# Performance work log

Hardware: AMD Instinct MI355X
Metric: run time of the kernel (lower is better)

Reference implementation:

```python
import jax, jax.numpy as jnp
import numpy as np

N_NODES = 100000
N_EDGES = 1600000
IN_C, HID_C, OUT_C, N_CLS = 64, 128, 64, 20


def setup_inputs() -> dict:
    key = jax.random.key(0)
    ks = jax.random.split(key, 8)
    s = lambda k, sh: jax.random.normal(k, sh, dtype=jnp.float32) * (1.0 / np.sqrt(sh[0]))
    return {
        "x": jax.random.normal(ks[0], (N_NODES, IN_C), dtype=jnp.float32),
        "edge_index": jax.random.randint(ks[1], (2, N_EDGES), 0, N_NODES, dtype=jnp.int64),
        "w_self1": s(ks[2], (IN_C, HID_C)),
        "w_neigh1": s(ks[3], (IN_C, HID_C)),
        "b1": jnp.zeros((HID_C,), dtype=jnp.float32),
        "w_self2": s(ks[4], (HID_C, OUT_C)),
        "w_neigh2": s(ks[5], (HID_C, OUT_C)),
        "b2": jnp.zeros((OUT_C,), dtype=jnp.float32),
        "wc": s(ks[6], (OUT_C, N_CLS)),
        "bc": jnp.zeros((N_CLS,), dtype=jnp.float32),
    }


def _sage_mean(feat, src, dst, deg_inv, w_self, w_neigh, b):
    # gather messages along edges, segment-sum at destinations, mean-normalize
    msg_sum = jax.ops.segment_sum(feat[src], dst, num_segments=N_NODES)  # [N, d]
    h_neigh = msg_sum * deg_inv[:, None]
    return feat @ w_self + h_neigh @ w_neigh + b


def reference(x, edge_index, w_self1, w_neigh1, b1, w_self2, w_neigh2, b2, wc, bc):
    src, dst = edge_index[0], edge_index[1]
    deg = jax.ops.segment_sum(jnp.ones((src.shape[0],), dtype=x.dtype), dst,
                              num_segments=N_NODES)
    deg_inv = 1.0 / jnp.maximum(deg, 1.0)  # zero-degree nodes -> 0 neighbor mean
    h = jax.nn.relu(_sage_mean(x, src, dst, deg_inv, w_self1, w_neigh1, b1))
    h = jax.nn.relu(_sage_mean(h, src, dst, deg_inv, w_self2, w_neigh2, b2))
    return h @ wc + bc
```

## Files before the change

### kernel.cpp

```cpp
#include <hip/hip_runtime.h>

#define N_NODES 100000
#define N_EDGES 1600000
#define IN_C    64
#define HID_C   128
#define OUT_C   64
#define N_CLS   20

#define BUCKETS 196
#define XSL     8
#define WCAP    2560
#define EPB     4096
#define CAPB    44

typedef __attribute__((ext_vector_type(8))) short short8;
typedef __attribute__((ext_vector_type(4))) float floatx4;

__device__ __forceinline__ unsigned short f2bf(float f) {
    union { float f; unsigned u; } v; v.f = f;
    unsigned r = v.u + 0x7FFFu + ((v.u >> 16) & 1u);
    return (unsigned short)(r >> 16);
}
__device__ __forceinline__ unsigned pk2(float lo, float hi) {
    return (unsigned)f2bf(lo) | ((unsigned)f2bf(hi) << 16);
}
__device__ __forceinline__ float bflo(unsigned w) { return __uint_as_float(w << 16); }
__device__ __forceinline__ float bfhi(unsigned w) { return __uint_as_float(w & 0xFFFF0000u); }

__global__ __launch_bounds__(256) void binA_kernel(
        const int* __restrict__ ei, int* __restrict__ bcnt,
        unsigned* __restrict__ bins)
{
    __shared__ unsigned lbins[BUCKETS * CAPB];
    __shared__ unsigned comp[EPB];
    __shared__ unsigned dsti[EPB];
    __shared__ int lcnt[BUCKETS], lofs[BUCKETS], gb[BUCKETS];
    __shared__ int sd[256];

    const int tid = threadIdx.x;
    const int xcd = blockIdx.x & (XSL - 1);
    const int e0  = blockIdx.x * EPB;

    for (int w = tid; w < BUCKETS; w += 256) lcnt[w] = 0;
    __syncthreads();

    for (int it = 0; it < EPB / 256; ++it) {
        int e = e0 + it * 256 + tid;
        if (e >= N_EDGES) break;
        int src = ei[e];
        int dst = ei[N_EDGES + e];
        int b = dst >> 9;
        unsigned pk = ((unsigned)(dst & 511) << 17) | (unsigned)src;
        int pos = atomicAdd(&lcnt[b], 1);
        if (pos < CAPB) {
            lbins[b * CAPB + pos] = pk;
        } else {
            int gp = atomicAdd(&bcnt[b * XSL + xcd], 1);
            if (gp < WCAP)
                bins[(unsigned)(b * XSL + xcd) * WCAP + gp] = pk;
        }
    }
    __syncthreads();

    int c = (tid < BUCKETS) ? min(lcnt[tid], CAPB) : 0;
    sd[tid] = c;
    __syncthreads();
    for (int off = 1; off < 256; off <<= 1) {
        int x = 0;
        if (tid >= off) x = sd[tid - off];
        __syncthreads();
        if (tid >= off) sd[tid] += x;
        __syncthreads();
    }
    if (tid < BUCKETS) lofs[tid] = sd[tid] - c;
    __syncthreads();
    const int T = sd[255];

    if (tid < BUCKETS) {
        int cw = min(lcnt[tid], CAPB);
        gb[tid] = (cw > 0) ? atomicAdd(&bcnt[tid * XSL + xcd], cw) : 0;
    }
    __syncthreads();

    if (tid < BUCKETS) {
        int cw = min(lcnt[tid], CAPB);
        int lo = lofs[tid];
        unsigned wb = (unsigned)(tid * XSL + xcd) * WCAP + (unsigned)gb[tid];
        for (int i = 0; i < cw; ++i) {
            comp[lo + i] = lbins[tid * CAPB + i];
            dsti[lo + i] = wb + i;
        }
    }
    __syncthreads();

    for (int i = tid; i < T; i += 256)
        bins[dsti[i]] = comp[i];
}

__global__ __launch_bounds__(256) void bscan_kernel(
        const int* __restrict__ bcnt, int* __restrict__ bucket_base,
        int* __restrict__ row_ptr)
{
    __shared__ int sd[256];
    int t = threadIdx.x;
    int tot = 0;
    if (t < BUCKETS) {
        for (int sl = 0; sl < XSL; ++sl)
            tot += min(bcnt[t * XSL + sl], WCAP);
    }
    sd[t] = tot;
    __syncthreads();
    for (int off = 1; off < 256; off <<= 1) {
        int x = 0;
        if (t >= off) x = sd[t - off];
        __syncthreads();
        if (t >= off) sd[t] += x;
        __syncthreads();
    }
    if (t < BUCKETS) bucket_base[t] = sd[t] - tot;
    if (t == 0) row_ptr[N_NODES] = N_EDGES;
}

__global__ __launch_bounds__(256) void buildB_kernel(
        const int* __restrict__ bcnt, const unsigned* __restrict__ bins,
        const int* __restrict__ bucket_base,
        int* __restrict__ row_ptr, int* __restrict__ sorted_src,
        float* __restrict__ dinv)
{
    __shared__ unsigned ent[16384];
    __shared__ int scnt[XSL], soff[XSL];
    __shared__ int cnt[512], lofs[512], cur[512];
    __shared__ int sd[256];

    const int b   = blockIdx.x;
    const int tid = threadIdx.x;
    const int node0 = b * 512;

    if (tid < XSL) scnt[tid] = min(bcnt[b * XSL + tid], WCAP);
    { int i = tid; cnt[i] = 0; cnt[i + 256] = 0; }
    __syncthreads();
    if (tid == 0) {
        int acc = 0;
        for (int sl = 0; sl < XSL; ++sl) {
            soff[sl] = acc;
            acc += scnt[sl];
            if (acc > 16384) { scnt[sl] -= (acc - 16384); acc = 16384; }
        }
    }
    __syncthreads();

    for (int sl = 0; sl < XSL; ++sl) {
        int len = scnt[sl];
        const unsigned* seg = bins + (unsigned)(b * XSL + sl) * WCAP;
        int base = soff[sl];
        for (int i = tid; i < len; i += 256) {
            unsigned e = seg[i];
            ent[base + i] = e;
            atomicAdd((unsigned*)&cnt[e >> 17], 1u);
        }
    }
    __syncthreads();
    const int T = soff[XSL - 1] + scnt[XSL - 1];

    int a0 = cnt[2 * tid], a1 = cnt[2 * tid + 1];
    int s2 = a0 + a1;
    sd[tid] = s2;
    __syncthreads();
    for (int off = 1; off < 256; off <<= 1) {
        int x = 0;
        if (tid >= off) x = sd[tid - off];
        __syncthreads();
        if (tid >= off) sd[tid] += x;
        __syncthreads();
    }
    int excl = sd[tid] - s2;
    lofs[2 * tid]     = excl;
    lofs[2 * tid + 1] = excl + a0;
    cur[2 * tid]      = excl;
    cur[2 * tid + 1]  = excl + a0;
    __syncthreads();

    const int gbase = bucket_base[b];
    for (int j = tid; j < 512; j += 256) {
        int node = node0 + j;
        if (node < N_NODES) {
            row_ptr[node] = gbase + lofs[j];
            dinv[node] = 1.0f / (float)max(cnt[j], 1);
        }
    }
    for (int i = tid; i < T; i += 256) {
        unsigned e = ent[i];
        int dl = e >> 17;
        int p = atomicAdd((unsigned*)&cur[dl], 1u);
        sorted_src[gbase + p] = (int)(e & 0x1FFFFu);
    }
}


__global__ __launch_bounds__(256) void cvt_x_kernel(
        const float* __restrict__ x, unsigned short* __restrict__ xb)
{
    int i = blockIdx.x * 256 + threadIdx.x;
    if (i >= N_NODES * 64 / 8) return;
    float4 a = ((const float4*)x)[(size_t)i * 2];
    float4 b = ((const float4*)x)[(size_t)i * 2 + 1];
    uint4 r;
    r.x = pk2(a.x, a.y); r.y = pk2(a.z, a.w);
    r.z = pk2(b.x, b.y); r.w = pk2(b.z, b.w);
    ((uint4*)xb)[i] = r;
}

__global__ __launch_bounds__(256) void prep_wt_kernel(
        const float* __restrict__ ws1, const float* __restrict__ wn1,
        const float* __restrict__ ws2, const float* __restrict__ wn2,
        unsigned short* __restrict__ wt1s, unsigned short* __restrict__ wt1n,
        unsigned short* __restrict__ wt2s, unsigned short* __restrict__ wt2n)
{
    int i = blockIdx.x * 256 + threadIdx.x;
    if (i < 8192) {
        int o = i >> 6, c = i & 63;
        wt1s[i] = f2bf(ws1[c * 128 + o]);
        wt1n[i] = f2bf(wn1[c * 128 + o]);
    } else if (i < 16384) {
        int j = i - 8192;
        int o = j >> 7, c = j & 127;
        wt2s[j] = f2bf(ws2[c * 64 + o]);
        wt2n[j] = f2bf(wn2[c * 64 + o]);
    }
}

__global__ __launch_bounds__(256) void gatherb_kernel(
        const int* __restrict__ row_ptr, const int* __restrict__ srcs,
        const unsigned short* __restrict__ featb,
        const float* __restrict__ dinv, unsigned short* __restrict__ aggb)
{
    int gid = blockIdx.x * 256 + threadIdx.x;
    int n = gid >> 3;
    int q = gid & 7;
    if (n >= N_NODES) return;
    int beg = row_ptr[n];
    int end = row_ptr[n + 1];
    const uint4* f4 = (const uint4*)featb;
    float a0=0,a1=0,a2=0,a3=0,a4=0,a5=0,a6=0,a7=0;
    int e = beg;
    for (; e + 4 <= end; e += 4) {
        int s0 = srcs[e], s1 = srcs[e+1], s2 = srcs[e+2], s3 = srcs[e+3];
        uint4 v0 = f4[(size_t)s0 * 8 + q];
        uint4 v1 = f4[(size_t)s1 * 8 + q];
        uint4 v2 = f4[(size_t)s2 * 8 + q];
        uint4 v3 = f4[(size_t)s3 * 8 + q];
        a0 += bflo(v0.x); a1 += bfhi(v0.x); a2 += bflo(v0.y); a3 += bfhi(v0.y);
        a4 += bflo(v0.z); a5 += bfhi(v0.z); a6 += bflo(v0.w); a7 += bfhi(v0.w);
        a0 += bflo(v1.x); a1 += bfhi(v1.x); a2 += bflo(v1.y); a3 += bfhi(v1.y);
        a4 += bflo(v1.z); a5 += bfhi(v1.z); a6 += bflo(v1.w); a7 += bfhi(v1.w);
        a0 += bflo(v2.x); a1 += bfhi(v2.x); a2 += bflo(v2.y); a3 += bfhi(v2.y);
        a4 += bflo(v2.z); a5 += bfhi(v2.z); a6 += bflo(v2.w); a7 += bfhi(v2.w);
        a0 += bflo(v3.x); a1 += bfhi(v3.x); a2 += bflo(v3.y); a3 += bfhi(v3.y);
        a4 += bflo(v3.z); a5 += bfhi(v3.z); a6 += bflo(v3.w); a7 += bfhi(v3.w);
    }
    for (; e < end; ++e) {
        uint4 v = f4[(size_t)srcs[e] * 8 + q];
        a0 += bflo(v.x); a1 += bfhi(v.x); a2 += bflo(v.y); a3 += bfhi(v.y);
        a4 += bflo(v.z); a5 += bfhi(v.z); a6 += bflo(v.w); a7 += bfhi(v.w);
    }
    float di = dinv[n];
    uint4 r;
    r.x = pk2(a0 * di, a1 * di);
    r.y = pk2(a2 * di, a3 * di);
    r.z = pk2(a4 * di, a5 * di);
    r.w = pk2(a6 * di, a7 * di);
    ((uint4*)aggb)[(size_t)n * 8 + q] = r;
}


__global__ __launch_bounds__(256) void dense1_mfma(
        const unsigned short* __restrict__ xb,
        const unsigned short* __restrict__ aggb,
        const unsigned short* __restrict__ wts,
        const unsigned short* __restrict__ wtn,
        const float* __restrict__ bias,
        unsigned short* __restrict__ h1b)
{
    int lane = threadIdx.x & 63;
    int wv   = threadIdx.x >> 6;
    int quad = lane >> 4;
    int col  = lane & 15;
    int nl = blockIdx.x * 64 + wv * 16 + col;
    int nc = min(nl, N_NODES - 1);
    bool ok = nl < N_NODES;

    const short8 bs0 = *(const short8*)(xb   + (size_t)nc * 64 +      quad * 8);
    const short8 bs1 = *(const short8*)(xb   + (size_t)nc * 64 + 32 + quad * 8);
    const short8 bn0 = *(const short8*)(aggb + (size_t)nc * 64 +      quad * 8);
    const short8 bn1 = *(const short8*)(aggb + (size_t)nc * 64 + 32 + quad * 8);

#pragma unroll
    for (int mt = 0; mt < 8; ++mt) {
        int m = mt * 16 + col;
        const short8 as0 = *(const short8*)(wts + (size_t)m * 64 +      quad * 8);
        const short8 as1 = *(const short8*)(wts + (size_t)m * 64 + 32 + quad * 8);
        const short8 an0 = *(const short8*)(wtn + (size_t)m * 64 +      quad * 8);
        const short8 an1 = *(const short8*)(wtn + (size_t)m * 64 + 32 + quad * 8);
        floatx4 acc = {0.f, 0.f, 0.f, 0.f};
        acc = __builtin_amdgcn_mfma_f32_16x16x32_bf16(as0, bs0, acc, 0, 0, 0);
        acc = __builtin_amdgcn_mfma_f32_16x16x32_bf16(as1, bs1, acc, 0, 0, 0);
        acc = __builtin_amdgcn_mfma_f32_16x16x32_bf16(an0, bn0, acc, 0, 0, 0);
        acc = __builtin_amdgcn_mfma_f32_16x16x32_bf16(an1, bn1, acc, 0, 0, 0);
        if (ok) {
            int och = mt * 16 + quad * 4;
            float4 bv = *(const float4*)(bias + och);
            ushort4 r;
            r.x = f2bf(fmaxf(acc[0] + bv.x, 0.f));
            r.y = f2bf(fmaxf(acc[1] + bv.y, 0.f));
            r.z = f2bf(fmaxf(acc[2] + bv.z, 0.f));
            r.w = f2bf(fmaxf(acc[3] + bv.w, 0.f));
            *(ushort4*)(h1b + (size_t)nl * 128 + och) = r;
        }
    }
}

__global__ __launch_bounds__(256) void t2_mfma(
        const unsigned short* __restrict__ h1b,
        const unsigned short* __restrict__ wtn,
        unsigned short* __restrict__ t2b)
{
    int lane = threadIdx.x & 63;
    int wv   = threadIdx.x >> 6;
    int quad = lane >> 4;
    int col  = lane & 15;
    int nl = blockIdx.x * 64 + wv * 16 + col;
    int nc = min(nl, N_NODES - 1);
    bool ok = nl < N_NODES;

    short8 b[4];
#pragma unroll
    for (int kc = 0; kc < 4; ++kc)
        b[kc] = *(const short8*)(h1b + (size_t)nc * 128 + kc * 32 + quad * 8);

#pragma unroll
    for (int mt = 0; mt < 4; ++mt) {
        int m = mt * 16 + col;
        floatx4 acc = {0.f, 0.f, 0.f, 0.f};
#pragma unroll
        for (int kc = 0; kc < 4; ++kc) {
            const short8 a = *(const short8*)(wtn + (size_t)m * 128 + kc * 32 + quad * 8);
            acc = __builtin_amdgcn_mfma_f32_16x16x32_bf16(a, b[kc], acc, 0, 0, 0);
        }
        if (ok) {
            int och = mt * 16 + quad * 4;
            ushort4 r;
            r.x = f2bf(acc[0]); r.y = f2bf(acc[1]);
            r.z = f2bf(acc[2]); r.w = f2bf(acc[3]);
            *(ushort4*)(t2b + (size_t)nl * 64 + och) = r;
        }
    }
}

__global__ __launch_bounds__(256) void dense2_cls_mfma(
        const unsigned short* __restrict__ h1b,
        const unsigned short* __restrict__ wts,
        const unsigned short* __restrict__ agg2b,
        const float* __restrict__ b2,
        const float* __restrict__ wc,
        const float* __restrict__ bc,
        float* __restrict__ out)
{
    __shared__ float hs[64][65];
    __shared__ float wcs[64 * N_CLS];
    __shared__ float bcs[N_CLS];

    int tid = threadIdx.x;
    int lane = tid & 63;
    int wv   = tid >> 6;
    int quad = lane >> 4;
    int col  = lane & 15;
    int node0 = blockIdx.x * 64;
    int nl = node0 + wv * 16 + col;
    int nc = min(nl, N_NODES - 1);

    for (int t = tid; t < 64 * N_CLS; t += 256) wcs[t] = wc[t];
    if (tid < N_CLS) bcs[tid] = bc[tid];

    short8 b[4];
#pragma unroll
    for (int kc = 0; kc < 4; ++kc)
        b[kc] = *(const short8*)(h1b + (size_t)nc * 128 + kc * 32 + quad * 8);

#pragma unroll
    for (int mt = 0; mt < 4; ++mt) {
        int m = mt * 16 + col;
        floatx4 acc = {0.f, 0.f, 0.f, 0.f};
#pragma unroll
        for (int kc = 0; kc < 4; ++kc) {
            const short8 a = *(const short8*)(wts + (size_t)m * 128 + kc * 32 + quad * 8);
            acc = __builtin_amdgcn_mfma_f32_16x16x32_bf16(a, b[kc], acc, 0, 0, 0);
        }
        int och = mt * 16 + quad * 4;
        ushort4 au = *(const ushort4*)(agg2b + (size_t)nc * 64 + och);
        float4 bv = *(const float4*)(b2 + och);
        hs[wv * 16 + col][och + 0] = fmaxf(acc[0] + __uint_as_float((unsigned)au.x << 16) + bv.x, 0.f);
        hs[wv * 16 + col][och + 1] = fmaxf(acc[1] + __uint_as_float((unsigned)au.y << 16) + bv.y, 0.f);
        hs[wv * 16 + col][och + 2] = fmaxf(acc[2] + __uint_as_float((unsigned)au.z << 16) + bv.z, 0.f);
        hs[wv * 16 + col][och + 3] = fmaxf(acc[3] + __uint_as_float((unsigned)au.w << 16) + bv.w, 0.f);
    }
    __syncthreads();

    for (int o = tid; o < 64 * N_CLS; o += 256) {
        int n = o / N_CLS, cls = o % N_CLS;
        if (node0 + n >= N_NODES) continue;
        float s = bcs[cls];
#pragma unroll
        for (int k = 0; k < 64; ++k) s += hs[n][k] * wcs[k * N_CLS + cls];
        out[(size_t)(node0 + n) * N_CLS + cls] = s;
    }
}


extern "C" void kernel_launch(void* const* d_in, const int* in_sizes, int n_in,
                              void* d_out, int out_size, void* d_ws, size_t ws_size,
                              hipStream_t stream)
{
    const float* x        = (const float*)d_in[0];
    const int*   ei       = (const int*)  d_in[1];
    const float* w_self1  = (const float*)d_in[2];
    const float* w_neigh1 = (const float*)d_in[3];
    const float* b1       = (const float*)d_in[4];
    const float* w_self2  = (const float*)d_in[5];
    const float* w_neigh2 = (const float*)d_in[6];
    const float* b2       = (const float*)d_in[7];
    const float* wc       = (const float*)d_in[8];
    const float* bc       = (const float*)d_in[9];
    float* out = (float*)d_out;

    const size_t N = N_NODES;
    int*      bcnt    = (int*)d_ws;
    int*      bbase   = bcnt + BUCKETS * XSL;
    int*      row_ptr = bbase + 200;
    unsigned* bins    = (unsigned*)(row_ptr + N + 8);
    int*      s_src   = (int*)(bins + BUCKETS * XSL * WCAP);
    float*    dinv    = (float*)(s_src + N_EDGES);
    unsigned short* xb    = (unsigned short*)(dinv + N);
    unsigned short* agg1b = xb + 64 * N;
    unsigned short* h1b   = agg1b + 64 * N;
    unsigned short* t2b   = h1b + 128 * N;
    unsigned short* agg2b = t2b + 64 * N;
    unsigned short* wt1s  = agg2b + 64 * N;
    unsigned short* wt1n  = wt1s + 8192;
    unsigned short* wt2s  = wt1n + 8192;
    unsigned short* wt2n  = wt2s + 8192;

    hipMemsetAsync(bcnt, 0, BUCKETS * XSL * sizeof(int), stream);

    const int EB2 = (N_EDGES + EPB - 1) / EPB;
    const int GB = (N_NODES * 8) / 256;
    const int MB = (N_NODES + 63) / 64;

    cvt_x_kernel<<<(N_NODES * 64 / 8 + 255) / 256, 256, 0, stream>>>(x, xb);
    prep_wt_kernel<<<64, 256, 0, stream>>>(w_self1, w_neigh1, w_self2, w_neigh2,
                                           wt1s, wt1n, wt2s, wt2n);

    binA_kernel<<<EB2, 256, 0, stream>>>(ei, bcnt, bins);
    bscan_kernel<<<1, 256, 0, stream>>>(bcnt, bbase, row_ptr);
    buildB_kernel<<<BUCKETS, 256, 0, stream>>>(bcnt, bins, bbase,
                                               row_ptr, s_src, dinv);

    gatherb_kernel<<<GB, 256, 0, stream>>>(row_ptr, s_src, xb, dinv, agg1b);
    dense1_mfma<<<MB, 256, 0, stream>>>(xb, agg1b, wt1s, wt1n, b1, h1b);
    t2_mfma<<<MB, 256, 0, stream>>>(h1b, wt2n, t2b);
    gatherb_kernel<<<GB, 256, 0, stream>>>(row_ptr, s_src, t2b, dinv, agg2b);
    dense2_cls_mfma<<<MB, 256, 0, stream>>>(h1b, wt2s, agg2b, b2, wc, bc, out);
}
```

Before: 325.7 us.

## Fuse gathers with dense MFMA stages and merge prologue and scan kernels

```diff
diff --git a/kernel.cpp b/kernel.cpp
--- a/kernel.cpp
+++ b/kernel.cpp
@@ -13,6 +13,8 @@
 #define EPB     4096
 #define CAPB    44
 
+#define CVT_BLOCKS 3125
+
 typedef __attribute__((ext_vector_type(8))) short short8;
 typedef __attribute__((ext_vector_type(4))) float floatx4;
 
@@ -26,6 +28,41 @@
 }
 __device__ __forceinline__ float bflo(unsigned w) { return __uint_as_float(w << 16); }
 __device__ __forceinline__ float bfhi(unsigned w) { return __uint_as_float(w & 0xFFFF0000u); }
+
+__global__ __launch_bounds__(256) void prologue_kernel(
+        const float* __restrict__ x,
+        const float* __restrict__ ws1, const float* __restrict__ wn1,
+        const float* __restrict__ ws2, const float* __restrict__ wn2,
+        unsigned short* __restrict__ xb,
+        unsigned short* __restrict__ wt1s, unsigned short* __restrict__ wt1n,
+        unsigned short* __restrict__ wt2s, unsigned short* __restrict__ wt2n,
+        int* __restrict__ bcnt)
+{
+    const int bid = blockIdx.x, tid = threadIdx.x;
+    if (bid < CVT_BLOCKS) {
+        int i = bid * 256 + tid;
+        float4 a = ((const float4*)x)[(size_t)i * 2];
+        float4 b = ((const float4*)x)[(size_t)i * 2 + 1];
+        uint4 r;
+        r.x = pk2(a.x, a.y); r.y = pk2(a.z, a.w);
+        r.z = pk2(b.x, b.y); r.w = pk2(b.z, b.w);
+        ((uint4*)xb)[i] = r;
+    } else if (bid == CVT_BLOCKS) {
+        for (int i = tid; i < BUCKETS * XSL; i += 256) bcnt[i] = 0;
+    } else {
+        int i = (bid - CVT_BLOCKS - 1) * 256 + tid;
+        if (i < 8192) {
+            int o = i >> 6, c = i & 63;
+            wt1s[i] = f2bf(ws1[c * 128 + o]);
+            wt1n[i] = f2bf(wn1[c * 128 + o]);
+        } else if (i < 16384) {
+            int j = i - 8192;
+            int o = j >> 7, c = j & 127;
+            wt2s[j] = f2bf(ws2[c * 64 + o]);
+            wt2n[j] = f2bf(wn2[c * 64 + o]);
+        }
+    }
+}
 
 __global__ __launch_bounds__(256) void binA_kernel(
         const int* __restrict__ ei, int* __restrict__ bcnt,
@@ -97,33 +134,8 @@
         bins[dsti[i]] = comp[i];
 }
 
-__global__ __launch_bounds__(256) void bscan_kernel(
-        const int* __restrict__ bcnt, int* __restrict__ bucket_base,
-        int* __restrict__ row_ptr)
-{
-    __shared__ int sd[256];
-    int t = threadIdx.x;
-    int tot = 0;
-    if (t < BUCKETS) {
-        for (int sl = 0; sl < XSL; ++sl)
-            tot += min(bcnt[t * XSL + sl], WCAP);
-    }
-    sd[t] = tot;
-    __syncthreads();
-    for (int off = 1; off < 256; off <<= 1) {
-        int x = 0;
-        if (t >= off) x = sd[t - off];
-        __syncthreads();
-        if (t >= off) sd[t] += x;
-        __syncthreads();
-    }
-    if (t < BUCKETS) bucket_base[t] = sd[t] - tot;
-    if (t == 0) row_ptr[N_NODES] = N_EDGES;
-}
-
 __global__ __launch_bounds__(256) void buildB_kernel(
         const int* __restrict__ bcnt, const unsigned* __restrict__ bins,
-        const int* __restrict__ bucket_base,
         int* __restrict__ row_ptr, int* __restrict__ sorted_src,
         float* __restrict__ dinv)
 {
@@ -131,10 +143,25 @@
     __shared__ int scnt[XSL], soff[XSL];
     __shared__ int cnt[512], lofs[512], cur[512];
     __shared__ int sd[256];
+    __shared__ int gbase_s;
 
     const int b   = blockIdx.x;
     const int tid = threadIdx.x;
     const int node0 = b * 512;
+
+    int part = 0;
+    for (int w = tid; w < b * XSL; w += 256) part += min(bcnt[w], WCAP);
+    sd[tid] = part;
+    __syncthreads();
+    for (int off = 128; off > 0; off >>= 1) {
+        if (tid < off) sd[tid] += sd[tid + off];
+        __syncthreads();
+    }
+    if (tid == 0) {
+        gbase_s = sd[0];
+        if (b == 0) row_ptr[N_NODES] = N_EDGES;
+    }
+    __syncthreads();
 
     if (tid < XSL) scnt[tid] = min(bcnt[b * XSL + tid], WCAP);
     { int i = tid; cnt[i] = 0; cnt[i + 256] = 0; }
@@ -180,7 +207,7 @@
     cur[2 * tid + 1]  = excl + a0;
     __syncthreads();
 
-    const int gbase = bucket_base[b];
+    const int gbase = gbase_s;
     for (int j = tid; j < 512; j += 256) {
         int node = node0 + j;
         if (node < N_NODES) {
@@ -196,212 +223,227 @@
     }
 }
 
-
-__global__ __launch_bounds__(256) void cvt_x_kernel(
-        const float* __restrict__ x, unsigned short* __restrict__ xb)
+__global__ __launch_bounds__(256, 4) void fused1_kernel(
+        const int* __restrict__ row_ptr, const int* __restrict__ srcs,
+        const unsigned short* __restrict__ xb,
+        const float* __restrict__ dinv,
+        const unsigned short* __restrict__ wt1s,
+        const unsigned short* __restrict__ wt1n,
+        const float* __restrict__ b1,
+        const unsigned short* __restrict__ wt2n,
+        unsigned short* __restrict__ h1b,
+        unsigned short* __restrict__ t2b)
 {
-    int i = blockIdx.x * 256 + threadIdx.x;
-    if (i >= N_NODES * 64 / 8) return;
-    float4 a = ((const float4*)x)[(size_t)i * 2];
-    float4 b = ((const float4*)x)[(size_t)i * 2 + 1];
-    uint4 r;
-    r.x = pk2(a.x, a.y); r.y = pk2(a.z, a.w);
-    r.z = pk2(b.x, b.y); r.w = pk2(b.z, b.w);
-    ((uint4*)xb)[i] = r;
-}
-
-__global__ __launch_bounds__(256) void prep_wt_kernel(
-        const float* __restrict__ ws1, const float* __restrict__ wn1,
-        const float* __restrict__ ws2, const float* __restrict__ wn2,
-        unsigned short* __restrict__ wt1s, unsigned short* __restrict__ wt1n,
-        unsigned short* __restrict__ wt2s, unsigned short* __restrict__ wt2n)
-{
-    int i = blockIdx.x * 256 + threadIdx.x;
-    if (i < 8192) {
-        int o = i >> 6, c = i & 63;
-        wt1s[i] = f2bf(ws1[c * 128 + o]);
-        wt1n[i] = f2bf(wn1[c * 128 + o]);
-    } else if (i < 16384) {
-        int j = i - 8192;
-        int o = j >> 7, c = j & 127;
-        wt2s[j] = f2bf(ws2[c * 64 + o]);
-        wt2n[j] = f2bf(wn2[c * 64 + o]);
-    }
-}
-
-__global__ __launch_bounds__(256) void gatherb_kernel(
-        const int* __restrict__ row_ptr, const int* __restrict__ srcs,
-        const unsigned short* __restrict__ featb,
-        const float* __restrict__ dinv, unsigned short* __restrict__ aggb)
-{
-    int gid = blockIdx.x * 256 + threadIdx.x;
-    int n = gid >> 3;
-    int q = gid & 7;
-    if (n >= N_NODES) return;
-    int beg = row_ptr[n];
-    int end = row_ptr[n + 1];
-    const uint4* f4 = (const uint4*)featb;
-    float a0=0,a1=0,a2=0,a3=0,a4=0,a5=0,a6=0,a7=0;
-    int e = beg;
-    for (; e + 4 <= end; e += 4) {
-        int s0 = srcs[e], s1 = srcs[e+1], s2 = srcs[e+2], s3 = srcs[e+3];
-        uint4 v0 = f4[(size_t)s0 * 8 + q];
-        uint4 v1 = f4[(size_t)s1 * 8 + q];
-        uint4 v2 = f4[(size_t)s2 * 8 + q];
-        uint4 v3 = f4[(size_t)s3 * 8 + q];
-        a0 += bflo(v0.x); a1 += bfhi(v0.x); a2 += bflo(v0.y); a3 += bfhi(v0.y);
-        a4 += bflo(v0.z); a5 += bfhi(v0.z); a6 += bflo(v0.w); a7 += bfhi(v0.w);
-        a0 += bflo(v1.x); a1 += bfhi(v1.x); a2 += bflo(v1.y); a3 += bfhi(v1.y);
-        a4 += bflo(v1.z); a5 += bfhi(v1.z); a6 += bflo(v1.w); a7 += bfhi(v1.w);
-        a0 += bflo(v2.x); a1 += bfhi(v2.x); a2 += bflo(v2.y); a3 += bfhi(v2.y);
-        a4 += bflo(v2.z); a5 += bfhi(v2.z); a6 += bflo(v2.w); a7 += bfhi(v2.w);
-        a0 += bflo(v3.x); a1 += bfhi(v3.x); a2 += bflo(v3.y); a3 += bfhi(v3.y);
-        a4 += bflo(v3.z); a5 += bfhi(v3.z); a6 += bflo(v3.w); a7 += bfhi(v3.w);
-    }
-    for (; e < end; ++e) {
-        uint4 v = f4[(size_t)srcs[e] * 8 + q];
-        a0 += bflo(v.x); a1 += bfhi(v.x); a2 += bflo(v.y); a3 += bfhi(v.y);
-        a4 += bflo(v.z); a5 += bfhi(v.z); a6 += bflo(v.w); a7 += bfhi(v.w);
-    }
-    float di = dinv[n];
-    uint4 r;
-    r.x = pk2(a0 * di, a1 * di);
-    r.y = pk2(a2 * di, a3 * di);
-    r.z = pk2(a4 * di, a5 * di);
-    r.w = pk2(a6 * di, a7 * di);
-    ((uint4*)aggb)[(size_t)n * 8 + q] = r;
-}
-
-
-__global__ __launch_bounds__(256) void dense1_mfma(
-        const unsigned short* __restrict__ xb,
-        const unsigned short* __restrict__ aggb,
-        const unsigned short* __restrict__ wts,
-        const unsigned short* __restrict__ wtn,
-        const float* __restrict__ bias,
-        unsigned short* __restrict__ h1b)
-{
-    int lane = threadIdx.x & 63;
-    int wv   = threadIdx.x >> 6;
-    int quad = lane >> 4;
-    int col  = lane & 15;
-    int nl = blockIdx.x * 64 + wv * 16 + col;
-    int nc = min(nl, N_NODES - 1);
-    bool ok = nl < N_NODES;
-
-    const short8 bs0 = *(const short8*)(xb   + (size_t)nc * 64 +      quad * 8);
-    const short8 bs1 = *(const short8*)(xb   + (size_t)nc * 64 + 32 + quad * 8);
-    const short8 bn0 = *(const short8*)(aggb + (size_t)nc * 64 +      quad * 8);
-    const short8 bn1 = *(const short8*)(aggb + (size_t)nc * 64 + 32 + quad * 8);
-
-#pragma unroll
-    for (int mt = 0; mt < 8; ++mt) {
-        int m = mt * 16 + col;
-        const short8 as0 = *(const short8*)(wts + (size_t)m * 64 +      quad * 8);
-        const short8 as1 = *(const short8*)(wts + (size_t)m * 64 + 32 + quad * 8);
-        const short8 an0 = *(const short8*)(wtn + (size_t)m * 64 +      quad * 8);
-        const short8 an1 = *(const short8*)(wtn + (size_t)m * 64 + 32 + quad * 8);
-        floatx4 acc = {0.f, 0.f, 0.f, 0.f};
-        acc = __builtin_amdgcn_mfma_f32_16x16x32_bf16(as0, bs0, acc, 0, 0, 0);
-        acc = __builtin_amdgcn_mfma_f32_16x16x32_bf16(as1, bs1, acc, 0, 0, 0);
-        acc = __builtin_amdgcn_mfma_f32_16x16x32_bf16(an0, bn0, acc, 0, 0, 0);
-        acc = __builtin_amdgcn_mfma_f32_16x16x32_bf16(an1, bn1, acc, 0, 0, 0);
-        if (ok) {
+    __shared__ unsigned short aggL[64 * 72];
+    __shared__ unsigned short h1L[64 * 136];
+
+    const int tid = threadIdx.x;
+    const int node0 = blockIdx.x * 64;
+
+    {
+        const int q  = tid & 7;
+        const int np = tid >> 3;
+        const uint4* f4 = (const uint4*)xb;
+        for (int half = 0; half < 2; ++half) {
+            int lrow = half * 32 + np;
+            int n = node0 + lrow;
+            float a0=0,a1=0,a2=0,a3=0,a4=0,a5=0,a6=0,a7=0;
+            if (n < N_NODES) {
+                int beg = row_ptr[n];
+                int end = row_ptr[n + 1];
+                int e = beg;
+                for (; e + 4 <= end; e += 4) {
+                    int s0 = srcs[e], s1 = srcs[e+1], s2 = srcs[e+2], s3 = srcs[e+3];
+                    uint4 v0 = f4[(size_t)s0 * 8 + q];
+                    uint4 v1 = f4[(size_t)s1 * 8 + q];
+                    uint4 v2 = f4[(size_t)s2 * 8 + q];
+                    uint4 v3 = f4[(size_t)s3 * 8 + q];
+                    a0 += bflo(v0.x); a1 += bfhi(v0.x); a2 += bflo(v0.y); a3 += bfhi(v0.y);
+                    a4 += bflo(v0.z); a5 += bfhi(v0.z); a6 += bflo(v0.w); a7 += bfhi(v0.w);
+                    a0 += bflo(v1.x); a1 += bfhi(v1.x); a2 += bflo(v1.y); a3 += bfhi(v1.y);
+                    a4 += bflo(v1.z); a5 += bfhi(v1.z); a6 += bflo(v1.w); a7 += bfhi(v1.w);
+                    a0 += bflo(v2.x); a1 += bfhi(v2.x); a2 += bflo(v2.y); a3 += bfhi(v2.y);
+                    a4 += bflo(v2.z); a5 += bfhi(v2.z); a6 += bflo(v2.w); a7 += bfhi(v2.w);
+                    a0 += bflo(v3.x); a1 += bfhi(v3.x); a2 += bflo(v3.y); a3 += bfhi(v3.y);
+                    a4 += bflo(v3.z); a5 += bfhi(v3.z); a6 += bflo(v3.w); a7 += bfhi(v3.w);
+                }
+                for (; e < end; ++e) {
+                    uint4 v = f4[(size_t)srcs[e] * 8 + q];
+                    a0 += bflo(v.x); a1 += bfhi(v.x); a2 += bflo(v.y); a3 += bfhi(v.y);
+                    a4 += bflo(v.z); a5 += bfhi(v.z); a6 += bflo(v.w); a7 += bfhi(v.w);
+                }
+                float di = dinv[n];
+                a0*=di; a1*=di; a2*=di; a3*=di; a4*=di; a5*=di; a6*=di; a7*=di;
+            }
+            uint4 r;
+            r.x = pk2(a0, a1); r.y = pk2(a2, a3);
+            r.z = pk2(a4, a5); r.w = pk2(a6, a7);
+            *(uint4*)(aggL + lrow * 72 + q * 8) = r;
+        }
+    }
+    __syncthreads();
+
+    const int lane = tid & 63;
+    const int wv   = tid >> 6;
+    const int quad = lane >> 4;
+    const int col  = lane & 15;
+    const int nrow = wv * 16 + col;
+    const int nl = node0 + nrow;
+    const int nc = min(nl, N_NODES - 1);
+    const bool ok = nl < N_NODES;
+
+    {
+        const short8 bs0 = *(const short8*)(xb + (size_t)nc * 64 +      quad * 8);
+        const short8 bs1 = *(const short8*)(xb + (size_t)nc * 64 + 32 + quad * 8);
+        const short8 bn0 = *(const short8*)(aggL + nrow * 72 +      quad * 8);
+        const short8 bn1 = *(const short8*)(aggL + nrow * 72 + 32 + quad * 8);
+
+#pragma unroll
+        for (int mt = 0; mt < 8; ++mt) {
+            int m = mt * 16 + col;
+            const short8 as0 = *(const short8*)(wt1s + (size_t)m * 64 +      quad * 8);
+            const short8 as1 = *(const short8*)(wt1s + (size_t)m * 64 + 32 + quad * 8);
+            const short8 an0 = *(const short8*)(wt1n + (size_t)m * 64 +      quad * 8);
+            const short8 an1 = *(const short8*)(wt1n + (size_t)m * 64 + 32 + quad * 8);
+            floatx4 acc = {0.f, 0.f, 0.f, 0.f};
+            acc = __builtin_amdgcn_mfma_f32_16x16x32_bf16(as0, bs0, acc, 0, 0, 0);
+            acc = __builtin_amdgcn_mfma_f32_16x16x32_bf16(as1, bs1, acc, 0, 0, 0);
+            acc = __builtin_amdgcn_mfma_f32_16x16x32_bf16(an0, bn0, acc, 0, 0, 0);
+            acc = __builtin_amdgcn_mfma_f32_16x16x32_bf16(an1, bn1, acc, 0, 0, 0);
             int och = mt * 16 + quad * 4;
-            float4 bv = *(const float4*)(bias + och);
+            float4 bv = *(const float4*)(b1 + och);
             ushort4 r;
             r.x = f2bf(fmaxf(acc[0] + bv.x, 0.f));
             r.y = f2bf(fmaxf(acc[1] + bv.y, 0.f));
             r.z = f2bf(fmaxf(acc[2] + bv.z, 0.f));
             r.w = f2bf(fmaxf(acc[3] + bv.w, 0.f));
-            *(ushort4*)(h1b + (size_t)nl * 128 + och) = r;
-        }
-    }
-}
-
-__global__ __launch_bounds__(256) void t2_mfma(
+            *(ushort4*)(h1L + nrow * 136 + och) = r;
+            if (ok) *(ushort4*)(h1b + (size_t)nl * 128 + och) = r;
+        }
+    }
+    __syncthreads();
+
+    {
+        short8 bfr[4];
+#pragma unroll
+        for (int kc = 0; kc < 4; ++kc)
+            bfr[kc] = *(const short8*)(h1L + nrow * 136 + kc * 32 + quad * 8);
+
+#pragma unroll
+        for (int mt = 0; mt < 4; ++mt) {
+            int m = mt * 16 + col;
+            floatx4 acc = {0.f, 0.f, 0.f, 0.f};
+#pragma unroll
+            for (int kc = 0; kc < 4; ++kc) {
+                const short8 a = *(const short8*)(wt2n + (size_t)m * 128 + kc * 32 + quad * 8);
+                acc = __builtin_amdgcn_mfma_f32_16x16x32_bf16(a, bfr[kc], acc, 0, 0, 0);
+            }
+            if (ok) {
+                int och = mt * 16 + quad * 4;
+                ushort4 r;
+                r.x = f2bf(acc[0]); r.y = f2bf(acc[1]);
+                r.z = f2bf(acc[2]); r.w = f2bf(acc[3]);
+                *(ushort4*)(t2b + (size_t)nl * 64 + och) = r;
+            }
+        }
+    }
+}
+
+__global__ __launch_bounds__(256, 4) void fused2_kernel(
+        const int* __restrict__ row_ptr, const int* __restrict__ srcs,
+        const unsigned short* __restrict__ t2b,
+        const float* __restrict__ dinv,
         const unsigned short* __restrict__ h1b,
-        const unsigned short* __restrict__ wtn,
-        unsigned short* __restrict__ t2b)
-{
-    int lane = threadIdx.x & 63;
-    int wv   = threadIdx.x >> 6;
-    int quad = lane >> 4;
-    int col  = lane & 15;
-    int nl = blockIdx.x * 64 + wv * 16 + col;
-    int nc = min(nl, N_NODES - 1);
-    bool ok = nl < N_NODES;
-
-    short8 b[4];
-#pragma unroll
-    for (int kc = 0; kc < 4; ++kc)
-        b[kc] = *(const short8*)(h1b + (size_t)nc * 128 + kc * 32 + quad * 8);
-
-#pragma unroll
-    for (int mt = 0; mt < 4; ++mt) {
-        int m = mt * 16 + col;
-        floatx4 acc = {0.f, 0.f, 0.f, 0.f};
-#pragma unroll
-        for (int kc = 0; kc < 4; ++kc) {
-            const short8 a = *(const short8*)(wtn + (size_t)m * 128 + kc * 32 + quad * 8);
-            acc = __builtin_amdgcn_mfma_f32_16x16x32_bf16(a, b[kc], acc, 0, 0, 0);
-        }
-        if (ok) {
-            int och = mt * 16 + quad * 4;
-            ushort4 r;
-            r.x = f2bf(acc[0]); r.y = f2bf(acc[1]);
-            r.z = f2bf(acc[2]); r.w = f2bf(acc[3]);
-            *(ushort4*)(t2b + (size_t)nl * 64 + och) = r;
-        }
-    }
-}
-
-__global__ __launch_bounds__(256) void dense2_cls_mfma(
-        const unsigned short* __restrict__ h1b,
-        const unsigned short* __restrict__ wts,
-        const unsigned short* __restrict__ agg2b,
+        const unsigned short* __restrict__ wt2s,
         const float* __restrict__ b2,
         const float* __restrict__ wc,
         const float* __restrict__ bc,
         float* __restrict__ out)
 {
+    __shared__ float aggL[64 * 68];
     __shared__ float hs[64][65];
     __shared__ float wcs[64 * N_CLS];
     __shared__ float bcs[N_CLS];
 
-    int tid = threadIdx.x;
-    int lane = tid & 63;
-    int wv   = tid >> 6;
-    int quad = lane >> 4;
-    int col  = lane & 15;
-    int node0 = blockIdx.x * 64;
-    int nl = node0 + wv * 16 + col;
-    int nc = min(nl, N_NODES - 1);
+    const int tid = threadIdx.x;
+    const int node0 = blockIdx.x * 64;
 
     for (int t = tid; t < 64 * N_CLS; t += 256) wcs[t] = wc[t];
     if (tid < N_CLS) bcs[tid] = bc[tid];
 
-    short8 b[4];
-#pragma unroll
-    for (int kc = 0; kc < 4; ++kc)
-        b[kc] = *(const short8*)(h1b + (size_t)nc * 128 + kc * 32 + quad * 8);
-
-#pragma unroll
-    for (int mt = 0; mt < 4; ++mt) {
-        int m = mt * 16 + col;
-        floatx4 acc = {0.f, 0.f, 0.f, 0.f};
-#pragma unroll
-        for (int kc = 0; kc < 4; ++kc) {
-            const short8 a = *(const short8*)(wts + (size_t)m * 128 + kc * 32 + quad * 8);
-            acc = __builtin_amdgcn_mfma_f32_16x16x32_bf16(a, b[kc], acc, 0, 0, 0);
-        }
-        int och = mt * 16 + quad * 4;
-        ushort4 au = *(const ushort4*)(agg2b + (size_t)nc * 64 + och);
-        float4 bv = *(const float4*)(b2 + och);
-        hs[wv * 16 + col][och + 0] = fmaxf(acc[0] + __uint_as_float((unsigned)au.x << 16) + bv.x, 0.f);
-        hs[wv * 16 + col][och + 1] = fmaxf(acc[1] + __uint_as_float((unsigned)au.y << 16) + bv.y, 0.f);
-        hs[wv * 16 + col][och + 2] = fmaxf(acc[2] + __uint_as_float((unsigned)au.z << 16) + bv.z, 0.f);
-        hs[wv * 16 + col][och + 3] = fmaxf(acc[3] + __uint_as_float((unsigned)au.w << 16) + bv.w, 0.f);
+    {
+        const int q  = tid & 7;
+        const int np = tid >> 3;
+        const uint4* f4 = (const uint4*)t2b;
+        for (int half = 0; half < 2; ++half) {
+            int lrow = half * 32 + np;
+            int n = node0 + lrow;
+            float a0=0,a1=0,a2=0,a3=0,a4=0,a5=0,a6=0,a7=0;
+            if (n < N_NODES) {
+                int beg = row_ptr[n];
+                int end = row_ptr[n + 1];
+                int e = beg;
+                for (; e + 4 <= end; e += 4) {
+                    int s0 = srcs[e], s1 = srcs[e+1], s2 = srcs[e+2], s3 = srcs[e+3];
+                    uint4 v0 = f4[(size_t)s0 * 8 + q];
+                    uint4 v1 = f4[(size_t)s1 * 8 + q];
+                    uint4 v2 = f4[(size_t)s2 * 8 + q];
+                    uint4 v3 = f4[(size_t)s3 * 8 + q];
+                    a0 += bflo(v0.x); a1 += bfhi(v0.x); a2 += bflo(v0.y); a3 += bfhi(v0.y);
+                    a4 += bflo(v0.z); a5 += bfhi(v0.z); a6 += bflo(v0.w); a7 += bfhi(v0.w);
+                    a0 += bflo(v1.x); a1 += bfhi(v1.x); a2 += bflo(v1.y); a3 += bfhi(v1.y);
+                    a4 += bflo(v1.z); a5 += bfhi(v1.z); a6 += bflo(v1.w); a7 += bfhi(v1.w);
+                    a0 += bflo(v2.x); a1 += bfhi(v2.x); a2 += bflo(v2.y); a3 += bfhi(v2.y);
+                    a4 += bflo(v2.z); a5 += bfhi(v2.z); a6 += bflo(v2.w); a7 += bfhi(v2.w);
+                    a0 += bflo(v3.x); a1 += bfhi(v3.x); a2 += bflo(v3.y); a3 += bfhi(v3.y);
+                    a4 += bflo(v3.z); a5 += bfhi(v3.z); a6 += bflo(v3.w); a7 += bfhi(v3.w);
+                }
+                for (; e < end; ++e) {
+                    uint4 v = f4[(size_t)srcs[e] * 8 + q];
+                    a0 += bflo(v.x); a1 += bfhi(v.x); a2 += bflo(v.y); a3 += bfhi(v.y);
+                    a4 += bflo(v.z); a5 += bfhi(v.z); a6 += bflo(v.w); a7 += bfhi(v.w);
+                }
+                float di = dinv[n];
+                a0*=di; a1*=di; a2*=di; a3*=di; a4*=di; a5*=di; a6*=di; a7*=di;
+            }
+            float* d = aggL + lrow * 68 + q * 8;
+            *(float4*)(d)     = make_float4(a0, a1, a2, a3);
+            *(float4*)(d + 4) = make_float4(a4, a5, a6, a7);
+        }
+    }
+    __syncthreads();
+
+    const int lane = tid & 63;
+    const int wv   = tid >> 6;
+    const int quad = lane >> 4;
+    const int col  = lane & 15;
+    const int nrow = wv * 16 + col;
+    const int nl = node0 + nrow;
+    const int nc = min(nl, N_NODES - 1);
+
+    {
+        short8 b[4];
+#pragma unroll
+        for (int kc = 0; kc < 4; ++kc)
+            b[kc] = *(const short8*)(h1b + (size_t)nc * 128 + kc * 32 + quad * 8);
+
+#pragma unroll
+        for (int mt = 0; mt < 4; ++mt) {
+            int m = mt * 16 + col;
+            floatx4 acc = {0.f, 0.f, 0.f, 0.f};
+#pragma unroll
+            for (int kc = 0; kc < 4; ++kc) {
+                const short8 a = *(const short8*)(wt2s + (size_t)m * 128 + kc * 32 + quad * 8);
+                acc = __builtin_amdgcn_mfma_f32_16x16x32_bf16(a, b[kc], acc, 0, 0, 0);
+            }
+            int och = mt * 16 + quad * 4;
+            float4 av = *(const float4*)(aggL + nrow * 68 + och);
+            float4 bv = *(const float4*)(b2 + och);
+            hs[nrow][och + 0] = fmaxf(acc[0] + av.x + bv.x, 0.f);
+            hs[nrow][och + 1] = fmaxf(acc[1] + av.y + bv.y, 0.f);
+            hs[nrow][och + 2] = fmaxf(acc[2] + av.z + bv.z, 0.f);
+            hs[nrow][och + 3] = fmaxf(acc[3] + av.w + bv.w, 0.f);
+        }
     }
     __syncthreads();
 
@@ -434,39 +476,29 @@
 
     const size_t N = N_NODES;
     int*      bcnt    = (int*)d_ws;
-    int*      bbase   = bcnt + BUCKETS * XSL;
-    int*      row_ptr = bbase + 200;
+    int*      row_ptr = bcnt + BUCKETS * XSL + 8;
     unsigned* bins    = (unsigned*)(row_ptr + N + 8);
     int*      s_src   = (int*)(bins + BUCKETS * XSL * WCAP);
     float*    dinv    = (float*)(s_src + N_EDGES);
     unsigned short* xb    = (unsigned short*)(dinv + N);
-    unsigned short* agg1b = xb + 64 * N;
-    unsigned short* h1b   = agg1b + 64 * N;
+    unsigned short* h1b   = xb + 64 * N;
     unsigned short* t2b   = h1b + 128 * N;
-    unsigned short* agg2b = t2b + 64 * N;
-    unsigned short* wt1s  = agg2b + 64 * N;
+    unsigned short* wt1s  = t2b + 64 * N;
     unsigned short* wt1n  = wt1s + 8192;
     unsigned short* wt2s  = wt1n + 8192;
     unsigned short* wt2n  = wt2s + 8192;
 
-    hipMemsetAsync(bcnt, 0, BUCKETS * XSL * sizeof(int), stream);
-
+    const int PB  = CVT_BLOCKS + 1 + 64;
     const int EB2 = (N_EDGES + EPB - 1) / EPB;
-    const int GB = (N_NODES * 8) / 256;
-    const int MB = (N_NODES + 63) / 64;
-
-    cvt_x_kernel<<<(N_NODES * 64 / 8 + 255) / 256, 256, 0, stream>>>(x, xb);
-    prep_wt_kernel<<<64, 256, 0, stream>>>(w_self1, w_neigh1, w_self2, w_neigh2,
-                                           wt1s, wt1n, wt2s, wt2n);
-
+    const int MB  = (N_NODES + 63) / 64;
+
+    prologue_kernel<<<PB, 256, 0, stream>>>(x, w_self1, w_neigh1, w_self2,
+                                            w_neigh2, xb, wt1s, wt1n, wt2s,
+                                            wt2n, bcnt);
     binA_kernel<<<EB2, 256, 0, stream>>>(ei, bcnt, bins);
-    bscan_kernel<<<1, 256, 0, stream>>>(bcnt, bbase, row_ptr);
-    buildB_kernel<<<BUCKETS, 256, 0, stream>>>(bcnt, bins, bbase,
-                                               row_ptr, s_src, dinv);
-
-    gatherb_kernel<<<GB, 256, 0, stream>>>(row_ptr, s_src, xb, dinv, agg1b);
-    dense1_mfma<<<MB, 256, 0, stream>>>(xb, agg1b, wt1s, wt1n, b1, h1b);
-    t2_mfma<<<MB, 256, 0, stream>>>(h1b, wt2n, t2b);
-    gatherb_kernel<<<GB, 256, 0, stream>>>(row_ptr, s_src, t2b, dinv, agg2b);
-    dense2_cls_mfma<<<MB, 256, 0, stream>>>(h1b, wt2s, agg2b, b2, wc, bc, out);
-}
+    buildB_kernel<<<BUCKETS, 256, 0, stream>>>(bcnt, bins, row_ptr, s_src, dinv);
+    fused1_kernel<<<MB, 256, 0, stream>>>(row_ptr, s_src, xb, dinv,
+                                          wt1s, wt1n, b1, wt2n, h1b, t2b);
+    fused2_kernel<<<MB, 256, 0, stream>>>(row_ptr, s_src, t2b, dinv,
+                                          h1b, wt2s, b2, wc, bc, out);
+}
```

Result: faster. 301.3 us (-7.5%).
